# Performance work log

Hardware: AMD Instinct MI355X
Metric: run time of the kernel (lower is better)

## Reference

```python
import jax, jax.numpy as jnp
import numpy as np

T, B = 21, 4096
H, E, V = 1024, 50, 96
PAD = 0


def setup_inputs() -> dict:
    key = jax.random.key(0)
    ks = jax.random.split(key, 10)
    s_e = 1.0 / np.sqrt(H)  # torch LSTM init scale
    emb = jax.random.normal(ks[0], (V, E), jnp.float32)
    emb = emb.at[PAD].set(0.0)  # padding_idx row is zero
    return {
        "input_ids": jax.random.randint(ks[1], (T, B), 0, V),
        "h0": jax.random.normal(ks[2], (1, B, H), jnp.float32),
        "c0": jax.random.normal(ks[3], (1, B, H), jnp.float32),
        "emb": emb,
        "W_ih": jax.random.uniform(ks[4], (4 * H, E), jnp.float32, -s_e, s_e),
        "W_hh": jax.random.uniform(ks[5], (4 * H, H), jnp.float32, -s_e, s_e),
        "b_ih": jax.random.uniform(ks[6], (4 * H,), jnp.float32, -s_e, s_e),
        "b_hh": jax.random.uniform(ks[7], (4 * H,), jnp.float32, -s_e, s_e),
        "W_out": jax.random.uniform(ks[8], (V, H), jnp.float32, -s_e, s_e),
        "b_out": jax.random.uniform(ks[9], (V,), jnp.float32, -s_e, s_e),
    }


def reference(input_ids, h0, c0, emb, W_ih, W_hh, b_ih, b_hh, W_out, b_out):
    # char_embeds: (T, B, E)
    x = emb[input_ids]
    # Precompute input projections for all timesteps in one GEMM: (T, B, 4H)
    x_proj = jnp.einsum("tbe,ge->tbg", x, W_ih) + b_ih + b_hh

    def step(carry, xp_t):
        h, c = carry  # (B, H) each
        gates = xp_t + h @ W_hh.T  # (B, 4H), torch gate order i,f,g,o
        i, f, g, o = jnp.split(gates, 4, axis=-1)
        i = jax.nn.sigmoid(i)
        f = jax.nn.sigmoid(f)
        g = jnp.tanh(g)
        o = jax.nn.sigmoid(o)
        c = f * c + i * g
        h = o * jnp.tanh(c)
        return (h, c), h

    (h_T, c_T), h_ts = jax.lax.scan(step, (h0[0], c0[0]), x_proj)
    # char_output_projection: (T, B, V)
    scores = jnp.einsum("tbh,vh->tbv", h_ts, W_out) + b_out
    return scores, (h_T[None], c_T[None])
```

## Files before the change

### kernel.cpp

```cpp
#include <hip/hip_runtime.h>
#include <hip/hip_bf16.h>


#define T_STEPS 21
#define BSZ 4096
#define HDIM 1024
#define VOCAB 96
#define EDIM 50

typedef __attribute__((ext_vector_type(8))) short short8;
typedef __attribute__((ext_vector_type(4))) short shortx4;
typedef __attribute__((ext_vector_type(4))) float f32x4;

#define GLL16(g, l)                                                        \
  __builtin_amdgcn_global_load_lds(                                        \
      (const __attribute__((address_space(1))) void*)(g),                  \
      (__attribute__((address_space(3))) void*)(l), 16, 0, 0)

#define ASM_BARRIER() asm volatile("s_barrier" ::: "memory")
#define ASM_VMCNT4() asm volatile("s_waitcnt vmcnt(4)" ::: "memory")
#define ASM_VMCNT0() asm volatile("s_waitcnt vmcnt(0)" ::: "memory")

__device__ __forceinline__ float sigmoidf_fast(float x) {
  return 1.0f / (1.0f + __expf(-x));
}
__device__ __forceinline__ float tanhf_fast(float x) {
  return 2.0f / (1.0f + __expf(-2.0f * x)) - 1.0f;
}
__device__ __forceinline__ float b2f(short s) {
  return __uint_as_float(((unsigned int)(unsigned short)s) << 16);
}

__global__ void prep_convert(const float* __restrict__ Whh_f,
                             const float* __restrict__ Wout_f,
                             const float* __restrict__ h0,
                             __hip_bfloat16* __restrict__ Whh,
                             __hip_bfloat16* __restrict__ Wout,
                             __hip_bfloat16* __restrict__ hb0) {
  int idx = blockIdx.x * 256 + threadIdx.x;
  if (idx < 4 * HDIM * HDIM) {
    Whh[idx] = __float2bfloat16(Whh_f[idx]);
    hb0[idx] = __float2bfloat16(h0[idx]);
  }
  if (idx < VOCAB * HDIM) Wout[idx] = __float2bfloat16(Wout_f[idx]);
}

__global__ void prep_ptable(const float* __restrict__ emb,
                            const float* __restrict__ Wih,
                            const float* __restrict__ bih,
                            const float* __restrict__ bhh,
                            __hip_bfloat16* __restrict__ Pb) {
  int idx = blockIdx.x * 256 + threadIdx.x;
  int v = idx >> 12, g = idx & 4095;
  int gate = g >> 10, j = g & 1023;
  const float* er = emb + v * EDIM;
  const float* wr = Wih + g * EDIM;
  float s = bih[g] + bhh[g];
#pragma unroll 10
  for (int e = 0; e < EDIM; ++e) s += er[e] * wr[e];
  Pb[(size_t)(j >> 6) * 24576 + v * 256 + (j & 63) * 4 + gate] =
      __float2bfloat16(s);
}


#define TILE(kk, CB, SB, DOSTAGE, VMW)                                     \
  {                                                                        \
    ASM_BARRIER();                                                         \
    const __hip_bfloat16* bufE =                                           \
        (const __hip_bfloat16*)(smem + (CB) * 32768);                      \
    short8 af[8], bf[4];                                                   \
    _Pragma("unroll") for (int mi = 0; mi < 8; ++mi)                       \
        af[mi] = *(const short8*)&bufE[a_off[mi]];                         \
    _Pragma("unroll") for (int g = 0; g < 4; ++g)                          \
        bf[g] = *(const short8*)&bufE[b_off[g]];                           \
    if (DOSTAGE) {                                                         \
      GLL16(hprev + aSrc[0] + ((kk) + 2) * 32,                             \
            smem + (SB) * 32768 + aDst0);                                  \
      GLL16(hprev + aSrc[1] + ((kk) + 2) * 32,                             \
            smem + (SB) * 32768 + aDst1);                                  \
      GLL16(Whh + bSrc[0] + ((kk) + 2) * 32,                               \
            smem + (SB) * 32768 + bDst0);                                  \
      GLL16(Whh + bSrc[1] + ((kk) + 2) * 32,                               \
            smem + (SB) * 32768 + bDst1);                                  \
    }                                                                      \
    __builtin_amdgcn_s_setprio(1);                                         \
    _Pragma("unroll") for (int mi = 0; mi < 8; ++mi)                       \
        _Pragma("unroll") for (int g = 0; g < 4; ++g)                      \
            acc[mi][g] = __builtin_amdgcn_mfma_f32_16x16x32_bf16(          \
                af[mi], bf[g], acc[mi][g], 0, 0, 0);                       \
    __builtin_amdgcn_s_setprio(0);                                         \
    VMW;                                                                   \
  }

template <bool LAST>
__global__ __launch_bounds__(512, 2) void lstm_step_kernel(
    const int* __restrict__ ids,
    const __hip_bfloat16* __restrict__ hprev,
    const __hip_bfloat16* __restrict__ Whh,
    const __hip_bfloat16* __restrict__ Pb,
    const float* __restrict__ c_in,
    float* __restrict__ c_out,
    __hip_bfloat16* __restrict__ hnext,
    float* __restrict__ hf32)
{
  __shared__ __align__(16) char smem[98304];

  const int tid = threadIdx.x;
  const int wid = tid >> 6;
  const int lane = tid & 63;
  const int wr = wid >> 2;
  const int wc = wid & 3;
  const int u16 = lane & 15;
  const int k16q = lane >> 4;

  const int bid = blockIdx.x;
  const int mt = (bid & 7) * 2 + ((bid >> 3) & 1);
  const int jt = bid >> 4;
  const int m0 = mt * 256;

  int a_off[8], b_off[4];
  {
    const int S = ((u16 & 1) << 2) | k16q;
#pragma unroll
    for (int mi = 0; mi < 8; ++mi) {
      const int La = wr * 64 + mi * 8 + (u16 >> 1);
      a_off[mi] = La * 64 + (S ^ (La & 7)) * 8;
    }
#pragma unroll
    for (int g = 0; g < 4; ++g) {
      const int Lb = wc * 32 + g * 8 + (u16 >> 1);
      b_off[g] = 8192 + Lb * 64 + (S ^ (Lb & 7)) * 8;
    }
  }

  size_t aSrc[2], bSrc[2];
  const int aDst0 = wid * 2048;
  const int aDst1 = wid * 2048 + 1024;
  const int bDst0 = 16384 + wid * 2048;
  const int bDst1 = 16384 + wid * 2048 + 1024;
  {
    const int lrow = lane >> 3;
    const int Sp = lane & 7;
#pragma unroll
    for (int q = 0; q < 2; ++q) {
      const int La = wid * 16 + q * 8 + lrow;
      const int S = Sp ^ (La & 7);
      const int arow = 2 * La + (S >> 2);
      aSrc[q] = (size_t)(m0 + arow) * HDIM + (S & 3) * 8;
      const int Lb = wid * 16 + q * 8 + lrow;
      const int S2 = Sp ^ (Lb & 7);
      const int n = 2 * Lb + (S2 >> 2);
      const int q4 = n >> 6, gate = (n >> 4) & 3, u = n & 15;
      bSrc[q] = (size_t)(gate * HDIM + jt * 64 + q4 * 16 + u) * HDIM +
                (S2 & 3) * 8;
    }
  }

  GLL16(hprev + aSrc[0], smem + aDst0);
  GLL16(hprev + aSrc[1], smem + aDst1);
  GLL16(Whh + bSrc[0], smem + bDst0);
  GLL16(Whh + bSrc[1], smem + bDst1);
  GLL16(hprev + aSrc[0] + 32, smem + 32768 + aDst0);
  GLL16(hprev + aSrc[1] + 32, smem + 32768 + aDst1);
  GLL16(Whh + bSrc[0] + 32, smem + 32768 + bDst0);
  GLL16(Whh + bSrc[1] + 32, smem + 32768 + bDst1);
  ASM_VMCNT4();

  f32x4 acc[8][4] = {};

#pragma unroll 1
  for (int kb = 0; kb < 30; kb += 3) {
    TILE(kb, 0, 2, true, ASM_VMCNT4());
    TILE(kb + 1, 1, 0, true, ASM_VMCNT4());
    TILE(kb + 2, 2, 1, true, ASM_VMCNT4());
  }
  TILE(30, 0, 0, false, ASM_VMCNT0());
  TILE(31, 1, 0, false, {});
  ASM_BARRIER();

  const int jcol = jt * 64 + wc * 16 + u16;
  float cpre[8][4];
#pragma unroll
  for (int mi = 0; mi < 8; ++mi)
#pragma unroll
    for (int r = 0; r < 4; ++r)
      cpre[mi][r] = c_in[(size_t)(m0 + wr * 128 + mi * 16 + k16q * 4 + r) *
                             HDIM +
                         jcol];

  {
    const __hip_bfloat16* Pbj = Pb + (size_t)jt * 24576;
#pragma unroll
    for (int i = 0; i < 6; ++i)
      GLL16(Pbj + (wid * 6 + i) * 512 + lane * 8,
            smem + (wid * 6 + i) * 1024);
  }
  ASM_VMCNT0();
  ASM_BARRIER();

  const __hip_bfloat16* sPb = (const __hip_bfloat16*)smem;
  const int uo4 = (wc * 16 + u16) * 4;
  const int rb = m0 + wr * 128 + k16q * 4;
#pragma unroll
  for (int mi = 0; mi < 8; ++mi) {
#pragma unroll
    for (int r = 0; r < 4; ++r) {
      const int row = rb + mi * 16 + r;
      const int id = ids[row];
      const shortx4 pv = *(const shortx4*)&sPb[id * 256 + uo4];
      float iv = acc[mi][0][r] + b2f(pv[0]);
      float fv = acc[mi][1][r] + b2f(pv[1]);
      float gv = acc[mi][2][r] + b2f(pv[2]);
      float ov = acc[mi][3][r] + b2f(pv[3]);
      iv = sigmoidf_fast(iv);
      fv = sigmoidf_fast(fv);
      gv = tanhf_fast(gv);
      ov = sigmoidf_fast(ov);
      const size_t off = (size_t)row * HDIM + jcol;
      const float cc = fv * cpre[mi][r] + iv * gv;
      c_out[off] = cc;
      const float hh = ov * tanhf_fast(cc);
      hnext[off] = __float2bfloat16(hh);
      if (LAST) hf32[off] = hh;
    }
  }
}

__global__ __launch_bounds__(256, 2) void scores_kernel(
    const __hip_bfloat16* __restrict__ h,
    const __hip_bfloat16* __restrict__ Wout,
    const float* __restrict__ bout,
    float* __restrict__ out)
{
  __shared__ __align__(16) __hip_bfloat16 sA[128 * 128];
  __shared__ __align__(16) __hip_bfloat16 sB[96 * 128];

  const int tid = threadIdx.x;
  const int wave = tid >> 6, lane = tid & 63;
  const int u16 = lane & 15, k16q = lane >> 4;
  const long r0 = (long)blockIdx.x * 128;

  f32x4 acc[2][6] = {};

  const int srow4 = lane >> 4;
  const int sslot = lane & 15;

  for (int k0 = 0; k0 < HDIM; k0 += 128) {
#pragma unroll
    for (int i = 0; i < 8; ++i) {
      int row = wave * 32 + i * 4 + srow4;
      int gg = sslot ^ (row & 15);
      GLL16(h + (r0 + row) * HDIM + k0 + gg * 8,
            &sA[(wave * 32 + i * 4) * 128]);
    }
#pragma unroll
    for (int i = 0; i < 6; ++i) {
      int row = wave * 24 + i * 4 + srow4;
      int gg = sslot ^ (row & 15);
      GLL16(Wout + (size_t)row * HDIM + k0 + gg * 8,
            &sB[(wave * 24 + i * 4) * 128]);
    }
    __syncthreads();
#pragma unroll
    for (int kk = 0; kk < 128; kk += 32) {
      const int sl = (((kk >> 3) + k16q) ^ u16) * 8;
      short8 af[2], bf[6];
#pragma unroll
      for (int mi = 0; mi < 2; ++mi)
        af[mi] = *(const short8*)&sA[(wave * 32 + mi * 16 + u16) * 128 + sl];
#pragma unroll
      for (int ni = 0; ni < 6; ++ni)
        bf[ni] = *(const short8*)&sB[(ni * 16 + u16) * 128 + sl];
#pragma unroll
      for (int mi = 0; mi < 2; ++mi)
#pragma unroll
        for (int ni = 0; ni < 6; ++ni)
          acc[mi][ni] = __builtin_amdgcn_mfma_f32_16x16x32_bf16(
              af[mi], bf[ni], acc[mi][ni], 0, 0, 0);
    }
    __syncthreads();
  }

#pragma unroll
  for (int ni = 0; ni < 6; ++ni) {
    int v = ni * 16 + u16;
    float bv = bout[v];
#pragma unroll
    for (int mi = 0; mi < 2; ++mi)
#pragma unroll
      for (int r = 0; r < 4; ++r) {
        long grow = r0 + wave * 32 + mi * 16 + k16q * 4 + r;
        out[grow * VOCAB + v] = acc[mi][ni][r] + bv;
      }
  }
}

extern "C" void kernel_launch(void* const* d_in, const int* in_sizes, int n_in,
                              void* d_out, int out_size, void* d_ws,
                              size_t ws_size, hipStream_t stream) {
  const int* ids = (const int*)d_in[0];
  const float* h0 = (const float*)d_in[1];
  const float* c0 = (const float*)d_in[2];
  const float* emb = (const float*)d_in[3];
  const float* Wih = (const float*)d_in[4];
  const float* Whh_f = (const float*)d_in[5];
  const float* bih = (const float*)d_in[6];
  const float* bhh = (const float*)d_in[7];
  const float* Wout_f = (const float*)d_in[8];
  const float* bout = (const float*)d_in[9];

  float* out = (float*)d_out;
  float* scores = out;
  float* hT = out + (size_t)T_STEPS * BSZ * VOCAB;
  float* cT = hT + (size_t)BSZ * HDIM;

  const size_t BH = (size_t)BSZ * HDIM;
  char* w = (char*)d_ws;
  __hip_bfloat16* Pb = (__hip_bfloat16*)w;   w += (size_t)16 * 24576 * 2;
  __hip_bfloat16* Whh = (__hip_bfloat16*)w;  w += (size_t)4 * HDIM * HDIM * 2;
  __hip_bfloat16* Wout = (__hip_bfloat16*)w; w += (size_t)VOCAB * HDIM * 2;
  __hip_bfloat16* hts = (__hip_bfloat16*)w;
  size_t base = (size_t)16 * 24576 * 2 + (size_t)4 * HDIM * HDIM * 2 +
                (size_t)VOCAB * HDIM * 2;
  const bool full = ws_size >= base + (size_t)(T_STEPS + 1) * BH * 2;

  prep_convert<<<dim3((4 * HDIM * HDIM + 255) / 256), dim3(256), 0, stream>>>(
      Whh_f, Wout_f, h0, Whh, Wout, hts);
  prep_ptable<<<dim3((VOCAB * 4096) / 256), dim3(256), 0, stream>>>(
      emb, Wih, bih, bhh, Pb);

  for (int t = 0; t < T_STEPS; ++t) {
    __hip_bfloat16* hp = hts + (full ? (size_t)t * BH : (size_t)(t & 1) * BH);
    __hip_bfloat16* hn =
        hts + (full ? (size_t)(t + 1) * BH : (size_t)((t + 1) & 1) * BH);
    const float* cin = (t == 0) ? c0 : cT;
    if (t == T_STEPS - 1) {
      lstm_step_kernel<true><<<dim3(256), dim3(512), 0, stream>>>(
          ids + (size_t)t * BSZ, hp, Whh, Pb, cin, cT, hn, hT);
    } else {
      lstm_step_kernel<false><<<dim3(256), dim3(512), 0, stream>>>(
          ids + (size_t)t * BSZ, hp, Whh, Pb, cin, cT, hn, nullptr);
    }
    if (!full) {
      scores_kernel<<<dim3(BSZ / 128), dim3(256), 0, stream>>>(
          hn, Wout, bout, scores + (size_t)t * BSZ * VOCAB);
    }
  }
  if (full) {
    scores_kernel<<<dim3(T_STEPS * BSZ / 128), dim3(256), 0, stream>>>(
        hts + BH, Wout, bout, scores);
  }
}
```

Baseline: 1.094 ms.

## Deepen LDS pipeline to four buffers and prefetch A fragments a tile ahead

Moves the recurrent GEMM's K-loop from a triple-buffered LDS ring with prefetch distance two to a four-buffer ring with distance three. It also loads the next tile's A fragments into registers during the current tile, so LDS reads overlap the MFMAs. Offsets are recomputed from a single base plus stride, replacing per-fragment offset arrays. This raises LDS to 128KB and adds register pressure. With launch_bounds(512,2) and 160KB of LDS per CU, it likely drops occupancy from two blocks per CU to one.

```diff
diff --git a/kernel.cpp b/kernel.cpp
--- a/kernel.cpp
+++ b/kernel.cpp
@@ -63,31 +63,35 @@
 }
 
 
-#define TILE(kk, CB, SB, DOSTAGE, VMW)                                     \
+#define TILE_RA(kk, CB, NB, AFC, AFN, RDNEXT, DOSTAGE, VMW)                \
   {                                                                        \
     ASM_BARRIER();                                                         \
-    const __hip_bfloat16* bufE =                                           \
+    const __hip_bfloat16* bufC =                                           \
         (const __hip_bfloat16*)(smem + (CB) * 32768);                      \
-    short8 af[8], bf[4];                                                   \
-    _Pragma("unroll") for (int mi = 0; mi < 8; ++mi)                       \
-        af[mi] = *(const short8*)&bufE[a_off[mi]];                         \
+    if (RDNEXT) {                                                          \
+      const __hip_bfloat16* bufN =                                         \
+          (const __hip_bfloat16*)(smem + (NB) * 32768);                    \
+      _Pragma("unroll") for (int mi = 0; mi < 8; ++mi)                     \
+          AFN[mi] = *(const short8*)&bufN[a_base + mi * 512];              \
+    }                                                                      \
+    short8 bf[4];                                                          \
     _Pragma("unroll") for (int g = 0; g < 4; ++g)                          \
-        bf[g] = *(const short8*)&bufE[b_off[g]];                           \
+        bf[g] = *(const short8*)&bufC[b_base + g * 512];                   \
     if (DOSTAGE) {                                                         \
-      GLL16(hprev + aSrc[0] + ((kk) + 2) * 32,                             \
-            smem + (SB) * 32768 + aDst0);                                  \
-      GLL16(hprev + aSrc[1] + ((kk) + 2) * 32,                             \
-            smem + (SB) * 32768 + aDst1);                                  \
-      GLL16(Whh + bSrc[0] + ((kk) + 2) * 32,                               \
-            smem + (SB) * 32768 + bDst0);                                  \
-      GLL16(Whh + bSrc[1] + ((kk) + 2) * 32,                               \
-            smem + (SB) * 32768 + bDst1);                                  \
+      GLL16(hprev + aSrc[0] + ((kk) + 3) * 32,                             \
+            smem + (((kk) + 3) & 3) * 32768 + aDst0);                      \
+      GLL16(hprev + aSrc[1] + ((kk) + 3) * 32,                             \
+            smem + (((kk) + 3) & 3) * 32768 + aDst1);                      \
+      GLL16(Whh + bSrc[0] + ((kk) + 3) * 32,                               \
+            smem + (((kk) + 3) & 3) * 32768 + bDst0);                      \
+      GLL16(Whh + bSrc[1] + ((kk) + 3) * 32,                               \
+            smem + (((kk) + 3) & 3) * 32768 + bDst1);                      \
     }                                                                      \
     __builtin_amdgcn_s_setprio(1);                                         \
-    _Pragma("unroll") for (int mi = 0; mi < 8; ++mi)                       \
-        _Pragma("unroll") for (int g = 0; g < 4; ++g)                      \
+    _Pragma("unroll") for (int g = 0; g < 4; ++g)                          \
+        _Pragma("unroll") for (int mi = 0; mi < 8; ++mi)                   \
             acc[mi][g] = __builtin_amdgcn_mfma_f32_16x16x32_bf16(          \
-                af[mi], bf[g], acc[mi][g], 0, 0, 0);                       \
+                AFC[mi], bf[g], acc[mi][g], 0, 0, 0);                      \
     __builtin_amdgcn_s_setprio(0);                                         \
     VMW;                                                                   \
   }
@@ -103,7 +107,7 @@
     __hip_bfloat16* __restrict__ hnext,
     float* __restrict__ hf32)
 {
-  __shared__ __align__(16) char smem[98304];
+  __shared__ __align__(16) char smem[131072];
 
   const int tid = threadIdx.x;
   const int wid = tid >> 6;
@@ -118,19 +122,12 @@
   const int jt = bid >> 4;
   const int m0 = mt * 256;
 
-  int a_off[8], b_off[4];
+  int a_base, b_base;
   {
     const int S = ((u16 & 1) << 2) | k16q;
-#pragma unroll
-    for (int mi = 0; mi < 8; ++mi) {
-      const int La = wr * 64 + mi * 8 + (u16 >> 1);
-      a_off[mi] = La * 64 + (S ^ (La & 7)) * 8;
-    }
-#pragma unroll
-    for (int g = 0; g < 4; ++g) {
-      const int Lb = wc * 32 + g * 8 + (u16 >> 1);
-      b_off[g] = 8192 + Lb * 64 + (S ^ (Lb & 7)) * 8;
-    }
+    const int hrow = u16 >> 1;
+    a_base = (wr * 64 + hrow) * 64 + (S ^ hrow) * 8;
+    b_base = 8192 + (wc * 32 + hrow) * 64 + (S ^ hrow) * 8;
   }
 
   size_t aSrc[2], bSrc[2];
@@ -147,35 +144,43 @@
       const int S = Sp ^ (La & 7);
       const int arow = 2 * La + (S >> 2);
       aSrc[q] = (size_t)(m0 + arow) * HDIM + (S & 3) * 8;
-      const int Lb = wid * 16 + q * 8 + lrow;
-      const int S2 = Sp ^ (Lb & 7);
-      const int n = 2 * Lb + (S2 >> 2);
+      const int n = 2 * La + (S >> 2);
       const int q4 = n >> 6, gate = (n >> 4) & 3, u = n & 15;
       bSrc[q] = (size_t)(gate * HDIM + jt * 64 + q4 * 16 + u) * HDIM +
-                (S2 & 3) * 8;
-    }
-  }
-
-  GLL16(hprev + aSrc[0], smem + aDst0);
-  GLL16(hprev + aSrc[1], smem + aDst1);
-  GLL16(Whh + bSrc[0], smem + bDst0);
-  GLL16(Whh + bSrc[1], smem + bDst1);
-  GLL16(hprev + aSrc[0] + 32, smem + 32768 + aDst0);
-  GLL16(hprev + aSrc[1] + 32, smem + 32768 + aDst1);
-  GLL16(Whh + bSrc[0] + 32, smem + 32768 + bDst0);
-  GLL16(Whh + bSrc[1] + 32, smem + 32768 + bDst1);
+                (S & 3) * 8;
+    }
+  }
+
+#pragma unroll
+  for (int t = 0; t < 3; ++t) {
+    GLL16(hprev + aSrc[0] + t * 32, smem + t * 32768 + aDst0);
+    GLL16(hprev + aSrc[1] + t * 32, smem + t * 32768 + aDst1);
+    GLL16(Whh + bSrc[0] + t * 32, smem + t * 32768 + bDst0);
+    GLL16(Whh + bSrc[1] + t * 32, smem + t * 32768 + bDst1);
+  }
   ASM_VMCNT4();
+  ASM_BARRIER();
 
   f32x4 acc[8][4] = {};
+  short8 afA[8], afB[8];
+  {
+    const __hip_bfloat16* buf0 = (const __hip_bfloat16*)smem;
+#pragma unroll
+    for (int mi = 0; mi < 8; ++mi)
+      afA[mi] = *(const short8*)&buf0[a_base + mi * 512];
+  }
 
 #pragma unroll 1
-  for (int kb = 0; kb < 30; kb += 3) {
-    TILE(kb, 0, 2, true, ASM_VMCNT4());
-    TILE(kb + 1, 1, 0, true, ASM_VMCNT4());
-    TILE(kb + 2, 2, 1, true, ASM_VMCNT4());
-  }
-  TILE(30, 0, 0, false, ASM_VMCNT0());
-  TILE(31, 1, 0, false, {});
+  for (int kb = 0; kb < 28; kb += 4) {
+    TILE_RA(kb + 0, 0, 1, afA, afB, true, true, ASM_VMCNT4());
+    TILE_RA(kb + 1, 1, 2, afB, afA, true, true, ASM_VMCNT4());
+    TILE_RA(kb + 2, 2, 3, afA, afB, true, true, ASM_VMCNT4());
+    TILE_RA(kb + 3, 3, 0, afB, afA, true, true, ASM_VMCNT4());
+  }
+  TILE_RA(28, 0, 1, afA, afB, true, true, ASM_VMCNT4());
+  TILE_RA(29, 1, 2, afB, afA, true, false, ASM_VMCNT0());
+  TILE_RA(30, 2, 3, afA, afB, true, false, {});
+  TILE_RA(31, 3, 0, afB, afA, false, false, {});
   ASM_BARRIER();
 
   const int jcol = jt * 64 + wc * 16 + u16;
```

New measurement: 1.117 ms. 1.02x slower.
